# Optimization experiments

Measured on AMD Instinct MI355X. Metric: run time of the kernel, lower is better.

Reference implementation:

```python
import jax, jax.numpy as jnp
import numpy as np

N = 50000      # nodes
E = 1600000    # edges (avg degree 32)
G = 128        # graphs in batch
NE = 5         # spectral supports (edge_attr channels)
NIN = 16       # input node features
H = 64         # nout1 hidden width
NCLS = 6
BN_EPS = 1e-5


def setup_inputs() -> dict:
    key = jax.random.key(0)
    ks = jax.random.split(key, 12)
    s = 0.1  # weight init scale
    x = jax.random.normal(ks[0], (N, NIN), dtype=jnp.float32)
    edge_index = jax.random.randint(ks[1], (2, E), 0, N, dtype=jnp.int32)
    edge_attr = jax.random.normal(ks[2], (E, NE), dtype=jnp.float32)
    # sorted segment ids covering all G graphs (non-empty segments)
    batch = ((jnp.arange(N, dtype=jnp.int32) * G) // N).astype(jnp.int32)
    W1 = jax.random.normal(ks[3], (NE, NIN, H), dtype=jnp.float32) * s
    W2 = jax.random.normal(ks[4], (NE, H, H), dtype=jnp.float32) * s
    W3 = jax.random.normal(ks[5], (NE, H, H), dtype=jnp.float32) * s
    W4 = jax.random.normal(ks[6], (NE, H, H), dtype=jnp.float32) * s
    b1 = jnp.zeros((H,), jnp.float32)
    b2 = jnp.zeros((H,), jnp.float32)
    b3 = jnp.zeros((H,), jnp.float32)
    b4 = jnp.zeros((H,), jnp.float32)
    bn_gamma = jnp.ones((2 * H,), jnp.float32)
    bn_beta = jnp.zeros((2 * H,), jnp.float32)
    bn_mean = jax.random.normal(ks[7], (2 * H,), dtype=jnp.float32)
    bn_var = jax.random.uniform(ks[8], (2 * H,), dtype=jnp.float32) + 0.5
    fc_w = jax.random.normal(ks[9], (2 * H, NCLS), dtype=jnp.float32) * s
    fc_b = jnp.zeros((NCLS,), jnp.float32)
    return {"x": x, "edge_index": edge_index, "edge_attr": edge_attr,
            "batch": batch, "W1": W1, "b1": b1, "W2": W2, "b2": b2,
            "W3": W3, "b3": b3, "W4": W4, "b4": b4,
            "bn_gamma": bn_gamma, "bn_beta": bn_beta,
            "bn_mean": bn_mean, "bn_var": bn_var,
            "fc_w": fc_w, "fc_b": fc_b}


def spect_conv(x, src, dst, edge_attr, W, b):
    # SpectConv(selfconn=False): out = sum_k scatter_add(edge_attr[:,k]*x[src] -> dst) @ W[k] + b
    xs = x[src]  # [E, F] gather
    n = x.shape[0]
    out = jnp.zeros((n, W.shape[2]), x.dtype)
    for k in range(W.shape[0]):  # K=5 spectral supports
        h = jax.ops.segment_sum(edge_attr[:, k:k + 1] * xs, dst, num_segments=n)
        out = out + h @ W[k]
    return out + b


def reference(x, edge_index, edge_attr, batch, W1, b1, W2, b2, W3, b3, W4, b4,
              bn_gamma, bn_beta, bn_mean, bn_var, fc_w, fc_b):
    src, dst = edge_index[0], edge_index[1]
    h = jax.nn.relu(spect_conv(x, src, dst, edge_attr, W1, b1))
    h = jax.nn.relu(spect_conv(h, src, dst, edge_attr, W2, b2))
    h = jax.nn.relu(spect_conv(h, src, dst, edge_attr, W3, b3))
    h = jax.nn.relu(spect_conv(h, src, dst, edge_attr, W4, b4))
    pooled = jnp.concatenate([
        jax.ops.segment_sum(h, batch, num_segments=G),
        jax.ops.segment_max(h, batch, num_segments=G)], axis=1)  # [G, 2H]
    bn = (pooled - bn_mean) * jax.lax.rsqrt(bn_var + BN_EPS) * bn_gamma + bn_beta
    return jax.nn.log_softmax(bn @ fc_w + fc_b, axis=1)
```

## Files before the change

### kernel.cpp

```cpp
#include <hip/hip_runtime.h>


#define Nn   50000
#define Ne   1600000
#define Gg   128
#define NEk  5
#define NINf 16
#define NCLSo 6
#define NB   196
#define RBK  128
#define CHK  (Ne / RBK)

using short8 = __attribute__((ext_vector_type(8))) short;
using f32x4  = __attribute__((ext_vector_type(4))) float;
using f32x2  = __attribute__((ext_vector_type(2))) float;

__device__ __forceinline__ float2 bf2u(unsigned u) {
    return make_float2(__uint_as_float(u << 16), __uint_as_float(u & 0xffff0000u));
}
__device__ __forceinline__ unsigned f2bf(float a, float b) {
    unsigned ua = __float_as_uint(a), ub = __float_as_uint(b);
    ua += 0x7fffu + ((ua >> 16) & 1u);
    ub += 0x7fffu + ((ub >> 16) & 1u);
    return (ua >> 16) | (ub & 0xffff0000u);
}
__device__ __forceinline__ unsigned short f2bf1(float a) {
    unsigned ua = __float_as_uint(a);
    ua += 0x7fffu + ((ua >> 16) & 1u);
    return (unsigned short)(ua >> 16);
}

__device__ __forceinline__ f32x2 fma2s(float a, f32x2 x, f32x2 c) {
#if __has_builtin(__builtin_elementwise_fma)
    f32x2 av; av.x = a; av.y = a;
    return __builtin_elementwise_fma(av, x, c);
#else
    c.x = fmaf(a, x.x, c.x); c.y = fmaf(a, x.y, c.y);
    return c;
#endif
}


__global__ void k_pad_x(const float* __restrict__ x, unsigned* __restrict__ h0) {
    int i = blockIdx.x * 256 + threadIdx.x;
    if (i >= Nn * 32) return;
    int n = i >> 5, p = i & 31;
    int f0 = 2 * p;
    float v0 = (f0 < NINf) ? x[n * NINf + f0] : 0.f;
    float v1 = (f0 + 1 < NINf) ? x[n * NINf + f0 + 1] : 0.f;
    h0[i] = f2bf(v0, v1);
}

__global__ void k_pad_w1(const float* __restrict__ W1, float* __restrict__ W1p) {
    int i = blockIdx.x * 256 + threadIdx.x;
    if (i >= NEk * 64 * 64) return;
    int h = i & 63, f = (i >> 6) & 63, k = i >> 12;
    W1p[i] = (f < NINf) ? W1[(k * NINf + f) * 64 + h] : 0.f;
}

__global__ void k_pack_b(const float* __restrict__ W, unsigned short* __restrict__ bhi,
                         unsigned short* __restrict__ blo) {
    int i = blockIdx.x * 256 + threadIdx.x;
    if (i >= 20480) return;
    int j = i & 7, lane = (i >> 3) & 63, t2 = i >> 9;
    int nt = t2 / 10, kstep = t2 - nt * 10;
    int k = kstep * 32 + (lane >> 4) * 8 + j;
    int col = nt * 16 + (lane & 15);
    float v = W[k * 64 + col];
    unsigned short hi = f2bf1(v);
    float fhi = __uint_as_float(((unsigned)hi) << 16);
    bhi[i] = hi;
    blo[i] = f2bf1(v - fhi);
}

__global__ __launch_bounds__(1024) void k_rankhist(
    const int* __restrict__ ei, unsigned short* __restrict__ lrank,
    unsigned short* __restrict__ cnt ) {
    __shared__ unsigned hist[12500];
    int b = blockIdx.x, t = threadIdx.x;
    int e0 = b * CHK;
    for (int w = t; w < 12500; w += 1024) hist[w] = 0;
    __syncthreads();
    for (int i = t; i < CHK; i += 1024) {
        int d = ei[Ne + e0 + i];
        unsigned sh = 8u * (unsigned)(d & 3);
        unsigned old = atomicAdd(&hist[d >> 2], 1u << sh);
        lrank[e0 + i] = (unsigned short)((old >> sh) & 0xffu);
    }
    __syncthreads();
    unsigned* co = (unsigned*)(cnt + (size_t)b * Nn);
    for (int w = t; w < 12500; w += 1024) {
        unsigned hv = hist[w];
        co[2 * w]     = (hv & 0xffu) | ((hv >> 8) & 0xffu) << 16;
        co[2 * w + 1] = ((hv >> 16) & 0xffu) | (hv >> 24) << 16;
    }
}

__global__ void k_colscan(unsigned short* __restrict__ cnt, int* __restrict__ deg) {
    int d = blockIdx.x * 256 + threadIdx.x;
    if (d >= Nn) return;
    int s = 0;
#pragma unroll 4
    for (int b = 0; b < RBK; ++b) {
        int t = cnt[(size_t)b * Nn + d];
        cnt[(size_t)b * Nn + d] = (unsigned short)s;
        s += t;
    }
    deg[d] = s;
}


__global__ void k_blocksum(const int* __restrict__ deg, int* __restrict__ bsum) {
    __shared__ int l[256];
    int t = threadIdx.x;
    int i = blockIdx.x * 256 + t;
    l[t] = (i < Nn) ? deg[i] : 0;
    __syncthreads();
    for (int off = 128; off > 0; off >>= 1) {
        if (t < off) l[t] += l[t + off];
        __syncthreads();
    }
    if (t == 0) bsum[blockIdx.x] = l[0];
}

__global__ void k_scanpart(const int* __restrict__ bsum, int* __restrict__ boff) {
    __shared__ int l[256];
    int t = threadIdx.x;
    int v = (t < NB) ? bsum[t] : 0;
    l[t] = v;
    __syncthreads();
    for (int off = 1; off < 256; off <<= 1) {
        int u = (t >= off) ? l[t - off] : 0;
        __syncthreads();
        l[t] += u;
        __syncthreads();
    }
    if (t < NB) boff[t] = l[t] - v;
}

__global__ void k_scanfinal(const int* __restrict__ deg, const int* __restrict__ boff,
                            int* __restrict__ rowstart) {
    __shared__ int l[256];
    int t = threadIdx.x;
    int i = blockIdx.x * 256 + t;
    int v = (i < Nn) ? deg[i] : 0;
    l[t] = v;
    __syncthreads();
    for (int off = 1; off < 256; off <<= 1) {
        int u = (t >= off) ? l[t - off] : 0;
        __syncthreads();
        l[t] += u;
        __syncthreads();
    }
    if (i <= Nn) rowstart[i] = boff[blockIdx.x] + l[t] - v;
}

__global__ void k_place(const int* __restrict__ ei, const float* __restrict__ eattr,
                        const int* __restrict__ rowstart,
                        const unsigned short* __restrict__ lrank,
                        const unsigned short* __restrict__ cnt,
                        uint4* __restrict__ recs) {
    int e = blockIdx.x * 256 + threadIdx.x;
    if (e >= Ne) return;
    int d = ei[Ne + e];
    int b = e / CHK;
    int pos = rowstart[d] + cnt[(size_t)b * Nn + d] + lrank[e];
    const float* a = eattr + (size_t)e * 5;
    uint4 rr;
    rr.x = (unsigned)ei[e];
    rr.y = f2bf(a[0], a[1]);
    rr.z = f2bf(a[2], a[3]);
    rr.w = f2bf(a[4], 0.f);
    recs[pos] = rr;
}

__global__ void k_bounds(const int* __restrict__ batch, int* __restrict__ sg,
                         int* __restrict__ eg) {
    int n = blockIdx.x * 256 + threadIdx.x;
    if (n >= Nn) return;
    int g = batch[n];
    if (n == 0) sg[g] = 0;
    else {
        int gp = batch[n - 1];
        if (gp != g) { sg[g] = n; eg[gp] = n; }
    }
    if (n == Nn - 1) eg[g] = Nn;
}


__global__ __launch_bounds__(256) void k_aggregate(
    const unsigned* __restrict__ hin, const int* __restrict__ rowstart,
    const uint4* __restrict__ recs, unsigned* __restrict__ agg) {
    int lane = threadIdx.x & 63;
    int l = lane & 31, half = lane >> 5;
    int node = __builtin_amdgcn_readfirstlane((int)(blockIdx.x * 4 + (threadIdx.x >> 6)));
    int beg = rowstart[node], end = rowstart[node + 1];
    f32x2 c0 = {0.f, 0.f}, c1 = c0, c2 = c0, c3 = c0, c4 = c0;
    int ee = beg;
#define EDGE(E) { \
    uint4 r = recs[(E)]; \
    unsigned hx = hin[(size_t)(int)r.x * 32 + l]; \
    f32x2 xv; xv.x = __uint_as_float(hx << 16); xv.y = __uint_as_float(hx & 0xffff0000u); \
    float A0 = __uint_as_float(r.y << 16), A1 = __uint_as_float(r.y & 0xffff0000u); \
    float A2 = __uint_as_float(r.z << 16), A3 = __uint_as_float(r.z & 0xffff0000u); \
    float A4 = __uint_as_float(r.w << 16); \
    c0 = fma2s(A0, xv, c0); c1 = fma2s(A1, xv, c1); \
    c2 = fma2s(A2, xv, c2); c3 = fma2s(A3, xv, c3); \
    c4 = fma2s(A4, xv, c4); }
    for (; ee + 8 <= end; ee += 8) {
        EDGE(ee + half) EDGE(ee + 2 + half) EDGE(ee + 4 + half) EDGE(ee + 6 + half)
    }
    for (; ee + 2 <= end; ee += 2) { EDGE(ee + half) }
    if (ee < end) { if (half == 0) { EDGE(ee) } }
#undef EDGE
    c0.x += __shfl(c0.x, lane ^ 32); c0.y += __shfl(c0.y, lane ^ 32);
    c1.x += __shfl(c1.x, lane ^ 32); c1.y += __shfl(c1.y, lane ^ 32);
    c2.x += __shfl(c2.x, lane ^ 32); c2.y += __shfl(c2.y, lane ^ 32);
    c3.x += __shfl(c3.x, lane ^ 32); c3.y += __shfl(c3.y, lane ^ 32);
    c4.x += __shfl(c4.x, lane ^ 32); c4.y += __shfl(c4.y, lane ^ 32);
    if (half == 0) {
        unsigned* o = agg + (size_t)node * 160 + l;
        o[0]   = f2bf(c0.x, c0.y);
        o[32]  = f2bf(c1.x, c1.y);
        o[64]  = f2bf(c2.x, c2.y);
        o[96]  = f2bf(c3.x, c3.y);
        o[128] = f2bf(c4.x, c4.y);
    }
}

#define SPAD 41
__global__ __launch_bounds__(256) void k_transform(
    const uint4* __restrict__ A, const unsigned short* __restrict__ bhi,
    const unsigned short* __restrict__ blo, const float* __restrict__ bias,
    unsigned* __restrict__ outh) {
    __shared__ uint4 smem[32 * SPAD];
    int t = threadIdx.x;
    int lane = t & 63, wave = t >> 6;
    int m = lane & 15, quad = lane >> 4;
    int blk = blockIdx.x;

#pragma unroll
    for (int it = 0; it < 5; ++it) {
        int v = t + it * 256;
        int row = v / 40, off = v - row * 40;
        int node = blk * 32 + row;
        if (node >= Nn) node = Nn - 1;
        smem[row * SPAD + off] = A[(size_t)node * 40 + off];
    }
    __syncthreads();

    f32x4 acc0 = {0.f, 0.f, 0.f, 0.f}, acc1 = acc0;
    const uint4* ar0 = smem + m * SPAD + quad;
    const uint4* ar1 = smem + (16 + m) * SPAD + quad;
    const size_t bbase = (size_t)wave * 5120;
#pragma unroll 2
    for (int ks = 0; ks < 10; ++ks) {
        short8 a0 = *(const short8*)(ar0 + ks * 4);
        short8 a1 = *(const short8*)(ar1 + ks * 4);
        size_t bb = bbase + ((size_t)ks * 64 + lane) * 8;
        short8 h = *(const short8*)(bhi + bb);
        short8 lo = *(const short8*)(blo + bb);
        acc0 = __builtin_amdgcn_mfma_f32_16x16x32_bf16(a0, h,  acc0, 0, 0, 0);
        acc0 = __builtin_amdgcn_mfma_f32_16x16x32_bf16(a0, lo, acc0, 0, 0, 0);
        acc1 = __builtin_amdgcn_mfma_f32_16x16x32_bf16(a1, h,  acc1, 0, 0, 0);
        acc1 = __builtin_amdgcn_mfma_f32_16x16x32_bf16(a1, lo, acc1, 0, 0, 0);
    }
    __syncthreads();

    float* Cs = (float*)smem;
#pragma unroll
    for (int r = 0; r < 4; ++r) {
        int base = (quad * 4 + r) * 72 + wave * 16 + m;
        Cs[base]            = acc0[r];
        Cs[base + 16 * 72]  = acc1[r];
    }
    __syncthreads();

    {
        int row = t >> 3, grp = t & 7;
        int node = blk * 32 + row;
        if (node < Nn) {
            const float* cr = Cs + row * 72;
            unsigned o[4];
#pragma unroll
            for (int j = 0; j < 4; ++j) {
                int pp = grp * 4 + j;
                float v0 = fmaxf(cr[2 * pp]     + bias[2 * pp],     0.f);
                float v1 = fmaxf(cr[2 * pp + 1] + bias[2 * pp + 1], 0.f);
                o[j] = f2bf(v0, v1);
            }
            *(uint4*)(outh + (size_t)node * 32 + grp * 4) =
                make_uint4(o[0], o[1], o[2], o[3]);
        }
    }
}


__global__ __launch_bounds__(256) void k_pool(const unsigned* __restrict__ h,
                                              const int* __restrict__ sg,
                                              const int* __restrict__ eg,
                                              float* __restrict__ pooled) {
    __shared__ float2 ls[256], lm[256];
    int g = blockIdx.x, t = threadIdx.x;
    int p = t & 31, q = t >> 5;
    int s = sg[g], e = eg[g];
    float2 sum = {0.f, 0.f}, mx = {0.f, 0.f};
    for (int n = s + q; n < e; n += 8) {
        float2 v = bf2u(h[(size_t)n * 32 + p]);
        sum.x += v.x; sum.y += v.y;
        mx.x = fmaxf(mx.x, v.x); mx.y = fmaxf(mx.y, v.y);
    }
    ls[t] = sum; lm[t] = mx;
    __syncthreads();
    if (t < 32) {
        float2 ss = ls[t], mm = lm[t];
        for (int i = 1; i < 8; ++i) {
            float2 a = ls[t + i * 32], b = lm[t + i * 32];
            ss.x += a.x; ss.y += a.y;
            mm.x = fmaxf(mm.x, b.x); mm.y = fmaxf(mm.y, b.y);
        }
        pooled[g * 128 + 2 * t]          = ss.x;
        pooled[g * 128 + 2 * t + 1]      = ss.y;
        pooled[g * 128 + 64 + 2 * t]     = mm.x;
        pooled[g * 128 + 64 + 2 * t + 1] = mm.y;
    }
}

__global__ void k_head(const float* __restrict__ pooled, const float* __restrict__ gamma,
                       const float* __restrict__ beta, const float* __restrict__ mean,
                       const float* __restrict__ var, const float* __restrict__ fcw,
                       const float* __restrict__ fcb, float* __restrict__ out) {
    __shared__ float y[128];
    __shared__ float lg[8];
    int g = blockIdx.x, c = threadIdx.x;
    float p = pooled[g * 128 + c];
    y[c] = (p - mean[c]) * rsqrtf(var[c] + 1e-5f) * gamma[c] + beta[c];
    __syncthreads();
    if (c < NCLSo) {
        float l = fcb[c];
        for (int i = 0; i < 128; ++i) l += y[i] * fcw[i * NCLSo + c];
        lg[c] = l;
    }
    __syncthreads();
    if (c == 0) {
        float m = lg[0];
        for (int j = 1; j < NCLSo; ++j) m = fmaxf(m, lg[j]);
        float se = 0.f;
        for (int j = 0; j < NCLSo; ++j) se += expf(lg[j] - m);
        float lse = m + logf(se);
        for (int j = 0; j < NCLSo; ++j) out[g * NCLSo + j] = lg[j] - lse;
    }
}


static inline size_t rup(size_t x) { return (x + 255) & ~(size_t)255; }

extern "C" void kernel_launch(void* const* d_in, const int* in_sizes, int n_in,
                              void* d_out, int out_size, void* d_ws, size_t ws_size,
                              hipStream_t stream) {
    const float* x     = (const float*)d_in[0];
    const int*   ei    = (const int*)d_in[1];
    const float* eattr = (const float*)d_in[2];
    const int*   batch = (const int*)d_in[3];
    const float* W1    = (const float*)d_in[4];
    const float* b1    = (const float*)d_in[5];
    const float* W2    = (const float*)d_in[6];
    const float* b2    = (const float*)d_in[7];
    const float* W3    = (const float*)d_in[8];
    const float* b3    = (const float*)d_in[9];
    const float* W4    = (const float*)d_in[10];
    const float* b4    = (const float*)d_in[11];
    const float* gamma = (const float*)d_in[12];
    const float* beta  = (const float*)d_in[13];
    const float* mean  = (const float*)d_in[14];
    const float* var   = (const float*)d_in[15];
    const float* fcw   = (const float*)d_in[16];
    const float* fcb   = (const float*)d_in[17];
    float* out = (float*)d_out;

    char* p = (char*)d_ws;
    auto take = [&](size_t bytes) { char* r = p; p += rup(bytes); return r; };
    int*            deg      = (int*)take((size_t)(Nn + 1) * 4);
    unsigned short* cnt      = (unsigned short*)take((size_t)RBK * Nn * 2);
    unsigned short* lrank    = (unsigned short*)take((size_t)Ne * 2);
    int*            rowstart = (int*)take((size_t)(Nn + 1) * 4);
    int*            bsum     = (int*)take((size_t)NB * 4);
    int*            boff     = (int*)take((size_t)NB * 4);
    uint4*          recs     = (uint4*)take((size_t)Ne * 16);
    unsigned*       hA       = (unsigned*)take((size_t)Nn * 32 * 4);
    unsigned*       hB       = (unsigned*)take((size_t)Nn * 32 * 4);
    unsigned*       agg      = (unsigned*)take((size_t)Nn * 160 * 4);
    float*          W1p      = (float*)take((size_t)NEk * 64 * 64 * 4);
    unsigned short* bhiA     = (unsigned short*)take((size_t)4 * 20480 * 2);
    unsigned short* bloA     = (unsigned short*)take((size_t)4 * 20480 * 2);
    float*          pooled   = (float*)take((size_t)Gg * 128 * 4);
    int*            sg       = (int*)take((size_t)Gg * 4);
    int*            eg       = (int*)take((size_t)Gg * 4);

    k_rankhist<<<RBK, 1024, 0, stream>>>(ei, lrank, cnt);
    k_pad_x<<<(Nn * 32 + 255) / 256, 256, 0, stream>>>(x, hA);
    k_pad_w1<<<(NEk * 64 * 64 + 255) / 256, 256, 0, stream>>>(W1, W1p);
    k_pack_b<<<80, 256, 0, stream>>>(W1p, bhiA,             bloA);
    k_pack_b<<<80, 256, 0, stream>>>(W2,  bhiA + 20480,     bloA + 20480);
    k_pack_b<<<80, 256, 0, stream>>>(W3,  bhiA + 2 * 20480, bloA + 2 * 20480);
    k_pack_b<<<80, 256, 0, stream>>>(W4,  bhiA + 3 * 20480, bloA + 3 * 20480);
    k_colscan<<<NB, 256, 0, stream>>>(cnt, deg);
    k_blocksum<<<NB, 256, 0, stream>>>(deg, bsum);
    k_scanpart<<<1, 256, 0, stream>>>(bsum, boff);
    k_scanfinal<<<NB, 256, 0, stream>>>(deg, boff, rowstart);
    k_place<<<(Ne + 255) / 256, 256, 0, stream>>>(ei, eattr, rowstart, lrank, cnt, recs);
    k_bounds<<<(Nn + 255) / 256, 256, 0, stream>>>(batch, sg, eg);

    const float* bs[4] = { b1, b2, b3, b4 };
    unsigned* cur = hA;
    unsigned* nxt = hB;
    for (int L = 0; L < 4; ++L) {
        k_aggregate<<<Nn / 4, 256, 0, stream>>>(cur, rowstart, recs, agg);
        k_transform<<<(Nn + 31) / 32, 256, 0, stream>>>(
            (const uint4*)agg, bhiA + (size_t)L * 20480, bloA + (size_t)L * 20480,
            bs[L], nxt);
        unsigned* tmp = cur; cur = nxt; nxt = tmp;
    }

    k_pool<<<Gg, 256, 0, stream>>>(cur, sg, eg, pooled);
    k_head<<<Gg, 128, 0, stream>>>(pooled, gamma, beta, mean, var, fcw, fcb, out);
}
```

Before: 455.9 us.

## Split aggregate feature halves across blocks, process four edges per wave iteration

The aggregate kernel now gives each node's 64 features to two blocks, each covering half of the feature words. Inside a wave, four 16-lane groups handle four edges at a time, where before two 32-lane halves handled two. Blocks are interleaved so the two feature halves of the same nodes run close together in time and can share edge-record reads in cache. This doubles the grid and the number of edge-record loads in exchange for more edges in flight per wave. It also adds a second shuffle reduction stage and a masked tail for leftover edges.

New measurement: 525.8 us. 1.15x slower.

```diff
diff --git a/kernel.cpp b/kernel.cpp
--- a/kernel.cpp
+++ b/kernel.cpp
@@ -192,34 +192,56 @@
     const unsigned* __restrict__ hin, const int* __restrict__ rowstart,
     const uint4* __restrict__ recs, unsigned* __restrict__ agg) {
     int lane = threadIdx.x & 63;
-    int l = lane & 31, half = lane >> 5;
-    int node = __builtin_amdgcn_readfirstlane((int)(blockIdx.x * 4 + (threadIdx.x >> 6)));
+    int w = lane & 15, slot = lane >> 4;
+    int blk = blockIdx.x;
+    int r = blk & 7, q = blk >> 3;
+    int fh = r >> 2;
+    int nb = q * 4 + (r & 3);
+    int node = __builtin_amdgcn_readfirstlane(nb * 4 + (int)(threadIdx.x >> 6));
     int beg = rowstart[node], end = rowstart[node + 1];
+    int fw = fh * 16 + w;
     f32x2 c0 = {0.f, 0.f}, c1 = c0, c2 = c0, c3 = c0, c4 = c0;
     int ee = beg;
-#define EDGE(E) { \
-    uint4 r = recs[(E)]; \
-    unsigned hx = hin[(size_t)(int)r.x * 32 + l]; \
+#define QEDGE(E) { \
+    uint4 rr = recs[(E) + slot]; \
+    unsigned hx = hin[(size_t)(int)rr.x * 32 + fw]; \
     f32x2 xv; xv.x = __uint_as_float(hx << 16); xv.y = __uint_as_float(hx & 0xffff0000u); \
-    float A0 = __uint_as_float(r.y << 16), A1 = __uint_as_float(r.y & 0xffff0000u); \
-    float A2 = __uint_as_float(r.z << 16), A3 = __uint_as_float(r.z & 0xffff0000u); \
-    float A4 = __uint_as_float(r.w << 16); \
+    float A0 = __uint_as_float(rr.y << 16), A1 = __uint_as_float(rr.y & 0xffff0000u); \
+    float A2 = __uint_as_float(rr.z << 16), A3 = __uint_as_float(rr.z & 0xffff0000u); \
+    float A4 = __uint_as_float(rr.w << 16); \
     c0 = fma2s(A0, xv, c0); c1 = fma2s(A1, xv, c1); \
     c2 = fma2s(A2, xv, c2); c3 = fma2s(A3, xv, c3); \
     c4 = fma2s(A4, xv, c4); }
-    for (; ee + 8 <= end; ee += 8) {
-        EDGE(ee + half) EDGE(ee + 2 + half) EDGE(ee + 4 + half) EDGE(ee + 6 + half)
-    }
-    for (; ee + 2 <= end; ee += 2) { EDGE(ee + half) }
-    if (ee < end) { if (half == 0) { EDGE(ee) } }
-#undef EDGE
+    for (; ee + 8 <= end; ee += 8) { QEDGE(ee) QEDGE(ee + 4) }
+    if (ee + 4 <= end) { QEDGE(ee) ee += 4; }
+    if (ee < end) {
+        int ei2 = ee + slot;
+        int val = ei2 < end;
+        if (!val) ei2 = end - 1;
+        uint4 rr = recs[ei2];
+        unsigned hx = hin[(size_t)(int)rr.x * 32 + fw];
+        f32x2 xv; xv.x = __uint_as_float(hx << 16); xv.y = __uint_as_float(hx & 0xffff0000u);
+        float msk = val ? 1.f : 0.f;
+        float A0 = __uint_as_float(rr.y << 16) * msk, A1 = __uint_as_float(rr.y & 0xffff0000u) * msk;
+        float A2 = __uint_as_float(rr.z << 16) * msk, A3 = __uint_as_float(rr.z & 0xffff0000u) * msk;
+        float A4 = __uint_as_float(rr.w << 16) * msk;
+        c0 = fma2s(A0, xv, c0); c1 = fma2s(A1, xv, c1);
+        c2 = fma2s(A2, xv, c2); c3 = fma2s(A3, xv, c3);
+        c4 = fma2s(A4, xv, c4);
+    }
+#undef QEDGE
+    c0.x += __shfl(c0.x, lane ^ 16); c0.y += __shfl(c0.y, lane ^ 16);
+    c1.x += __shfl(c1.x, lane ^ 16); c1.y += __shfl(c1.y, lane ^ 16);
+    c2.x += __shfl(c2.x, lane ^ 16); c2.y += __shfl(c2.y, lane ^ 16);
+    c3.x += __shfl(c3.x, lane ^ 16); c3.y += __shfl(c3.y, lane ^ 16);
+    c4.x += __shfl(c4.x, lane ^ 16); c4.y += __shfl(c4.y, lane ^ 16);
     c0.x += __shfl(c0.x, lane ^ 32); c0.y += __shfl(c0.y, lane ^ 32);
     c1.x += __shfl(c1.x, lane ^ 32); c1.y += __shfl(c1.y, lane ^ 32);
     c2.x += __shfl(c2.x, lane ^ 32); c2.y += __shfl(c2.y, lane ^ 32);
     c3.x += __shfl(c3.x, lane ^ 32); c3.y += __shfl(c3.y, lane ^ 32);
     c4.x += __shfl(c4.x, lane ^ 32); c4.y += __shfl(c4.y, lane ^ 32);
-    if (half == 0) {
-        unsigned* o = agg + (size_t)node * 160 + l;
+    if (slot == 0) {
+        unsigned* o = agg + (size_t)node * 160 + fw;
         o[0]   = f2bf(c0.x, c0.y);
         o[32]  = f2bf(c1.x, c1.y);
         o[64]  = f2bf(c2.x, c2.y);
@@ -415,7 +437,7 @@
     unsigned* cur = hA;
     unsigned* nxt = hB;
     for (int L = 0; L < 4; ++L) {
-        k_aggregate<<<Nn / 4, 256, 0, stream>>>(cur, rowstart, recs, agg);
+        k_aggregate<<<2 * (Nn / 4), 256, 0, stream>>>(cur, rowstart, recs, agg);
         k_transform<<<(Nn + 31) / 32, 256, 0, stream>>>(
             (const uint4*)agg, bhiA + (size_t)L * 20480, bloA + (size_t)L * 20480,
             bs[L], nxt);
```
